# Kernel tuning notes

Measured on AMD Instinct MI355X. Metric: run time of the kernel, lower is better.

Reference implementation:

```python
import jax, jax.numpy as jnp
import numpy as np

M = 41
RHO = 4.0
HDIM = 10
NMODES = 2
BATCH = 16384


def triplet_index(m_size, rho):
    # reduced PBC triplet index set: n >= m, |m|,|n|,|m+n| <= (M-1)/2, |m*n| <= rho*(M-1)/2
    h = (m_size - 1) // 2
    idx = [(m, n) for m in range(-h, h + 1) for n in range(m, h + 1)
           if abs(m + n) <= h and abs(m * n) <= rho * h]
    return np.array(idx, dtype=np.int32)

IDX = triplet_index(M, RHO)
S = len(IDX)


def _c(a):
    # last-dim-2 real tensor -> complex
    return jax.lax.complex(a[..., 0], a[..., 1])


def setup_inputs() -> dict:
    key = jax.random.key(0)
    ks = jax.random.split(key, 6)
    x = jax.random.normal(ks[0], (BATCH, M, NMODES, 2), dtype=jnp.float32)
    task_info = jax.random.uniform(ks[1], (BATCH, 4), dtype=jnp.float32)  # col 0 = power in dBm
    pbc_C = 0.01 * jax.random.normal(ks[2], (S, 2), dtype=jnp.float32)  # complex PBC coeffs
    W1 = jax.random.normal(ks[3], (HDIM, NMODES, S, 2), dtype=jnp.float32) / np.sqrt(2.0 * NMODES * S)
    b1 = jnp.zeros((HDIM, 2), dtype=jnp.float32)
    W2 = jax.random.normal(ks[4], (HDIM, NMODES, M, 2), dtype=jnp.float32) / np.sqrt(2.0 * NMODES * M)
    b2 = jnp.zeros((HDIM, 2), dtype=jnp.float32)
    m_idx = jnp.asarray(IDX[:, 0], dtype=jnp.int32)
    n_idx = jnp.asarray(IDX[:, 1], dtype=jnp.int32)
    return {"x": x, "task_info": task_info, "pbc_C": pbc_C,
            "W1": W1, "b1": b1, "W2": W2, "b2": b2,
            "m_idx": m_idx, "n_idx": n_idx}


def _nonlinear_features(E, m_idx, n_idx):
    # E: [B, M, 2] complex -> [B, 2, S]; Manakov dual-pol triplets:
    # F[p] = (E[c+m,p]*conj(E[c+m+n,p]) + E[c+m,q]*conj(E[c+m+n,q])) * E[c+n,p]
    c = E.shape[1] // 2
    A = E[:, c + m_idx, :] * jnp.conj(E[:, c + m_idx + n_idx, :])  # [B, S, 2]
    F = (A + A[..., ::-1]) * E[:, c + n_idx, :]                    # [B, S, 2]
    return jnp.transpose(F, (0, 2, 1))                             # [B, 2, S]


def _conv_full(Wc, bc, inp):
    # ComplexConv1d whose kernel spans the whole input length (output length 1) -> [B, out]
    return jnp.einsum('oik,bik->bo', Wc, inp) + bc


def _forward(x, task_info, pbc_C, W1, b1, W2, b2, m_idx, n_idx):
    E = _c(x)                                    # [B, M, 2] complex64
    c = M // 2
    P = 10.0 ** (task_info[:, 0] / 10.0) / NMODES  # [B] launch power per mode
    F = _nonlinear_features(E, m_idx, n_idx)     # [B, 2, S]
    # EqAMPBC: center symbol + P * (triplet features . complex coeffs)
    pbc_out = E[:, c, :] + P[:, None] * jnp.einsum('bps,s->bp', F, _c(pbc_C))  # [B, 2]
    w1, bb1, w2, bb2 = _c(W1), _c(b1), _c(W2), _c(b2)
    # A = cat([f1(fo), f1(fo with pols flipped)], dim=-1) -> [B, hdim, 2]
    A = jnp.stack([_conv_full(w1, bb1, F), _conv_full(w1, bb1, F[:, ::-1, :])], axis=-1)
    Et = jnp.transpose(E, (0, 2, 1))             # [B, 2, M]
    Bm = jnp.stack([_conv_full(w2, bb2, Et), _conv_full(w2, bb2, Et[:, ::-1, :])], axis=-1)
    term = jnp.sum(A * Bm * jnp.conj(Bm) + jnp.conj(A) * Bm * Bm, axis=1)  # [B, 2]
    out = pbc_out + (1e-4 / np.sqrt(HDIM)) * term * (P[:, None] ** 2)
    return jnp.stack([out.real, out.imag], axis=-1)  # [B, 2, 2] float32


def reference(x, task_info, pbc_C, W1, b1, W2, b2, m_idx, n_idx):
    return _forward(x, task_info, pbc_C, W1, b1, W2, b2, m_idx, n_idx)
```

## Files before the change

### kernel.cpp

```cpp
#include <hip/hip_runtime.h>
#include <hip/hip_bf16.h>

typedef short bf16x8 __attribute__((ext_vector_type(8)));
typedef float f32x16 __attribute__((ext_vector_type(16)));
typedef float f32x4  __attribute__((ext_vector_type(4)));
typedef float f32x2  __attribute__((ext_vector_type(2)));

#define NCOL  32
#define KS1   112
#define KS2   12
#define ESTR  528

#define WP_OFF   0
#define W2P_OFF  229376

#define MET_OFF  21648
#define SUM_OFF  25360
#define SUM2_OFF 41744
#define LDS_BYTES 58128

__device__ __forceinline__ unsigned short f2bf(float f) {
    union { float f; unsigned u; } v; v.f = f;
    unsigned r = v.u + 0x7FFFu + ((v.u >> 16) & 1u);
    return (unsigned short)(r >> 16);
}
__device__ __forceinline__ unsigned pk2(float a, float b) {
    __hip_bfloat162 h = __float22bfloat162_rn(make_float2(a, b));
    unsigned u; __builtin_memcpy(&u, &h, 4); return u;
}
__device__ __forceinline__ bf16x8 asbf(uint4 v) {
    union { uint4 u; bf16x8 b; } z; z.u = v; return z.b;
}
__device__ __forceinline__ f32x16 zero16() {
    f32x16 z;
#pragma unroll
    for (int i = 0; i < 16; ++i) z[i] = 0.f;
    return z;
}

__global__ void prep_kernel(const float* __restrict__ W1,
                            const float* __restrict__ W2,
                            const float* __restrict__ pbcC,
                            unsigned short* __restrict__ Wp,
                            unsigned short* __restrict__ W2p, int S) {
    int idx = blockIdx.x * 256 + threadIdx.x;
    const int N1 = KS1 * 2 * 64 * 2;
    const int N2 = KS2 * 2 * 64 * 2;
    if (idx < N1) {
        int ks = idx >> 8, rem = idx & 255;
        int mt = rem >> 7; rem &= 127;
        int lane = rem >> 1, jh = rem & 1;
        int row = mt * 32 + (lane & 31);
        int kg  = ks * 16 + (lane >> 5) * 8 + jh * 4;
        int s   = kg >> 2;
        float2 wj0 = make_float2(0.f, 0.f), wj1 = make_float2(0.f, 0.f);
        int p = 0, r = 0;
        if (s < S) {
            if (row < 40) {
                int o = row >> 2; p = (row >> 1) & 1; r = row & 1;
                wj0 = ((const float2*)W1)[(size_t)(o * 2 + 0) * S + s];
                wj1 = ((const float2*)W1)[(size_t)(o * 2 + 1) * S + s];
            } else if (row < 44) {
                p = (row >> 1) & 1; r = row & 1;
                wj0 = ((const float2*)pbcC)[s];
            }
        }
        ushort4 h; unsigned short us[4];
#pragma unroll
        for (int t = 0; t < 4; ++t) {
            int i = t & 1, cc = t >> 1, j2 = i ^ p;
            float2 w = j2 ? wj1 : wj0;
            float v = (cc == 0) ? (r ? w.y : w.x) : (r ? w.x : -w.y);
            us[t] = f2bf(v);
        }
        h.x = us[0]; h.y = us[1]; h.z = us[2]; h.w = us[3];
        ((ushort4*)Wp)[idx] = h;
        return;
    }
    idx -= N1;
    if (idx < N2) {
        int ks = idx >> 8, rem = idx & 255;
        int mt = rem >> 7; rem &= 127;
        int lane = rem >> 1, jh = rem & 1;
        int row = mt * 32 + (lane & 31);
        int kg  = ks * 16 + (lane >> 5) * 8 + jh * 4;
        int m   = kg >> 2;
        float2 wj0 = make_float2(0.f, 0.f), wj1 = make_float2(0.f, 0.f);
        int p = 0, r = 0;
        if (m < 41 && row < 40) {
            int o = row >> 2; p = (row >> 1) & 1; r = row & 1;
            wj0 = ((const float2*)W2)[(o * 2 + 0) * 41 + m];
            wj1 = ((const float2*)W2)[(o * 2 + 1) * 41 + m];
        }
        ushort4 h; unsigned short us[4];
#pragma unroll
        for (int t = 0; t < 4; ++t) {
            int i = t & 1, cc = t >> 1, j2 = i ^ p;
            float2 w = j2 ? wj1 : wj0;
            float v = (cc == 0) ? (r ? w.y : w.x) : (r ? w.x : -w.y);
            us[t] = f2bf(v);
        }
        h.x = us[0]; h.y = us[1]; h.z = us[2]; h.w = us[3];
        ((ushort4*)W2p)[idx] = h;
    }
}

__global__ __launch_bounds__(512, 4) void eqsonn_kernel(
    const float* __restrict__ x, const float* __restrict__ task,
    const unsigned short* __restrict__ Wp,
    const unsigned short* __restrict__ W2p,
    const int* __restrict__ m_idx, const int* __restrict__ n_idx,
    const float* __restrict__ b1, const float* __restrict__ b2,
    float* __restrict__ out, int B, int S)
{
    __shared__ alignas(16) char ldsb[LDS_BYTES];
    const int tid  = threadIdx.x;
    const int lane = tid & 63;
    const int w    = __builtin_amdgcn_readfirstlane(tid >> 6);
    const int col  = lane & 31;
    const int kha  = lane >> 5;
    const int b0   = blockIdx.x * NCOL;

    for (int e = tid; e < 41 * NCOL; e += 512) {
        int bb = e / 41, k = e - bb * 41;
        int bs = b0 + bb; if (bs > B - 1) bs = B - 1;
        float4 v = ((const float4*)x)[(size_t)bs * 41 + k];
        f32x4 pv; pv.x = v.x; pv.y = v.z; pv.z = v.y; pv.w = v.w;
        *(f32x4*)(ldsb + k * ESTR + bb * 16) = pv;
    }
    if (tid < 464) {
        int m = 0, n = 0;
        if (tid < S) { m = m_idx[tid]; n = n_idx[tid]; }
        unsigned offM = (unsigned)((20 + m) * ESTR);
        unsigned offB = (unsigned)((20 + m + n) * ESTR);
        unsigned offN = (unsigned)((20 + n) * ESTR);
        *(uint2*)(ldsb + MET_OFF + tid * 8) = make_uint2(offM | (offB << 16), offN);
    }
    __syncthreads();

    const char* Ebase = ldsb + col * 16;
    auto ldM4 = [&](int ks) -> uint4 {
        return *(const uint4*)(ldsb + MET_OFF + (ks * 4 + kha * 2) * 8);
    };
    auto ldE = [&](unsigned off) -> f32x4 {
        return *(const f32x4*)(Ebase + off);
    };
    auto fbuild = [&](f32x4 em, f32x4 eq, f32x4 en, unsigned& lo, unsigned& hi) {
        f32x2 mr = em.xy, mi = em.zw;
        f32x2 qr = eq.xy, qi = eq.zw;
        f32x2 nr = en.xy, ni = en.zw;
        f32x2 t = mr * qr + mi * qi;
        f32x2 u = mi * qr - mr * qi;
        float sr = t.x + t.y, si = u.x + u.y;
        f32x2 Fr = sr * nr - si * ni;
        f32x2 Fi = sr * ni + si * nr;
        lo = pk2(Fr.x, Fr.y); hi = pk2(Fi.x, Fi.y);
    };

    f32x16 ac0 = zero16(), ac1 = zero16();
    {
        const int ks0 = w * 14;
        const short* Wp16 = (const short*)Wp;
        uint4 M = ldM4(ks0);
        f32x4 e0 = ldE(M.x & 0xffffu), e1 = ldE(M.x >> 16), e2 = ldE(M.y);
        f32x4 e3 = ldE(M.z & 0xffffu), e4 = ldE(M.z >> 16), e5 = ldE(M.w);
        uint4 Mc = ldM4(ks0 + 1);
        const short* ap0 = Wp16 + (size_t)ks0 * 1024 + lane * 8;
        bf16x8 A0 = *(const bf16x8*)(ap0);
        bf16x8 A1 = *(const bf16x8*)(ap0 + 512);
        for (int ks = ks0; ks < ks0 + 14; ++ks) {
            int ksn = (ks + 1 < KS1) ? ks + 1 : KS1 - 1;
            const short* apn = Wp16 + (size_t)ksn * 1024 + lane * 8;
            bf16x8 N0 = *(const bf16x8*)(apn);
            bf16x8 N1 = *(const bf16x8*)(apn + 512);
            f32x4 f0 = ldE(Mc.x & 0xffffu), f1v = ldE(Mc.x >> 16), f2v = ldE(Mc.y);
            f32x4 f3 = ldE(Mc.z & 0xffffu), f4v = ldE(Mc.z >> 16), f5v = ldE(Mc.w);
            uint4 Mn = ldM4(ks + 2);
            unsigned g0, g1, g2, g3;
            fbuild(e0, e1, e2, g0, g1);
            fbuild(e3, e4, e5, g2, g3);
            bf16x8 bfr = asbf(make_uint4(g0, g1, g2, g3));
            ac0 = __builtin_amdgcn_mfma_f32_32x32x16_bf16(A0, bfr, ac0, 0, 0, 0);
            ac1 = __builtin_amdgcn_mfma_f32_32x32x16_bf16(A1, bfr, ac1, 0, 0, 0);
            e0 = f0; e1 = f1v; e2 = f2v; e3 = f3; e4 = f4v; e5 = f5v; Mc = Mn;
            A0 = N0; A1 = N1;
        }
    }

    f32x16 bc0 = zero16(), bc1 = zero16();
    {
        const short* W216 = (const short*)W2p;
        for (int ks2 = w; ks2 < KS2; ks2 += 8) {
            const short* ap = W216 + (size_t)ks2 * 1024 + lane * 8;
            bf16x8 A0 = *(const bf16x8*)(ap);
            bf16x8 A1 = *(const bf16x8*)(ap + 512);
            unsigned g[4];
#pragma unroll
            for (int j = 0; j < 2; ++j) {
                int m = ks2 * 4 + kha * 2 + j;
                int mc = m < 41 ? m : 40;
                f32x4 v = *(const f32x4*)(ldsb + mc * ESTR + col * 16);
                unsigned lo = pk2(v.x, v.y);
                unsigned hi = pk2(v.z, v.w);
                if (m >= 41) { lo = 0u; hi = 0u; }
                g[j * 2] = lo; g[j * 2 + 1] = hi;
            }
            bf16x8 bfr = asbf(make_uint4(g[0], g[1], g[2], g[3]));
            bc0 = __builtin_amdgcn_mfma_f32_32x32x16_bf16(A0, bfr, bc0, 0, 0, 0);
            bc1 = __builtin_amdgcn_mfma_f32_32x32x16_bf16(A1, bfr, bc1, 0, 0, 0);
        }
    }

    float* Reg = (float*)(ldsb + ((w < 4) ? SUM_OFF : SUM2_OFF));
    const int ph = w & 3;
    auto dump = [&](f32x16 a, int baserow, bool add) {
#pragma unroll
        for (int reg = 0; reg < 16; ++reg) {
            int row = baserow + (reg & 3) + 8 * (reg >> 2) + 4 * kha;
            int idx = row * 32 + col;
            if (add) Reg[idx] += a[reg]; else Reg[idx] = a[reg];
        }
    };
    for (int p = 0; p < 4; ++p) {
        if (ph == p) {
            bool add = (p != 0);
            dump(ac0, 0, add); dump(ac1, 32, add);
            dump(bc0, 64, add); dump(bc1, 96, add);
        }
        __syncthreads();
    }

    {
        float4* S1 = (float4*)(ldsb + SUM_OFF);
        float4* S2 = (float4*)(ldsb + SUM2_OFF);
#pragma unroll
        for (int i = 0; i < 2; ++i) {
            int idx = tid + i * 512;
            float4 a = S1[idx], b = S2[idx];
            a.x += b.x; a.y += b.y; a.z += b.z; a.w += b.w;
            S1[idx] = a;
        }
    }
    __syncthreads();

    if (w == 0 && lane < NCOL) {
        const float* Sum = (const float*)(ldsb + SUM_OFF);
        int c = lane;
        float pr0 = Sum[40 * 32 + c], pi0 = Sum[41 * 32 + c];
        float pr1 = Sum[42 * 32 + c], pi1 = Sum[43 * 32 + c];
        float t0 = 0.f, t1 = 0.f, t2 = 0.f, t3 = 0.f;
#pragma unroll
        for (int o = 0; o < 10; ++o) {
            float b2r = b2[o * 2], b2i = b2[o * 2 + 1];
            float b1r = b1[o * 2], b1i = b1[o * 2 + 1];
            int rb = o * 4;
            float B0r = Sum[(64 + rb + 0) * 32 + c] + b2r;
            float B0i = Sum[(64 + rb + 1) * 32 + c] + b2i;
            float B1r = Sum[(64 + rb + 2) * 32 + c] + b2r;
            float B1i = Sum[(64 + rb + 3) * 32 + c] + b2i;
            float A0r = Sum[(rb + 0) * 32 + c] + b1r;
            float A0i = Sum[(rb + 1) * 32 + c] + b1i;
            float A1r = Sum[(rb + 2) * 32 + c] + b1r;
            float A1i = Sum[(rb + 3) * 32 + c] + b1i;
            float g0 = 2.f * (A0r * B0r + A0i * B0i);
            t0 += g0 * B0r; t1 += g0 * B0i;
            float g1 = 2.f * (A1r * B1r + A1i * B1i);
            t2 += g1 * B1r; t3 += g1 * B1i;
        }
        int b = b0 + c;
        if (b < B) {
            float dbm = task[(size_t)b * 4];
            float P   = exp2f(dbm * 0.33219280948873623f) * 0.5f;
            float kP2 = 3.1622776601683794e-05f * P * P;
            float4 Ec = ((const float4*)x)[(size_t)b * 41 + 20];
            float4 o4;
            o4.x = Ec.x + P * pr0 + kP2 * t0;
            o4.y = Ec.y + P * pi0 + kP2 * t1;
            o4.z = Ec.z + P * pr1 + kP2 * t2;
            o4.w = Ec.w + P * pi1 + kP2 * t3;
            ((float4*)out)[b] = o4;
        }
    }
}

extern "C" void kernel_launch(void* const* d_in, const int* in_sizes, int n_in,
                              void* d_out, int out_size, void* d_ws, size_t ws_size,
                              hipStream_t stream) {
    const float* x     = (const float*)d_in[0];
    const float* task  = (const float*)d_in[1];
    const float* pbcC  = (const float*)d_in[2];
    const float* W1    = (const float*)d_in[3];
    const float* b1    = (const float*)d_in[4];
    const float* W2    = (const float*)d_in[5];
    const float* b2    = (const float*)d_in[6];
    const int*   m_idx = (const int*)d_in[7];
    const int*   n_idx = (const int*)d_in[8];
    float* out = (float*)d_out;

    int S = in_sizes[7];
    int B = in_sizes[0] / (41 * 2 * 2);

    char* ws = (char*)d_ws;
    unsigned short* Wp  = (unsigned short*)(ws + WP_OFF);
    unsigned short* W2p = (unsigned short*)(ws + W2P_OFF);

    int prep_n = KS1 * 2 * 64 * 2 + KS2 * 2 * 64 * 2;
    prep_kernel<<<(prep_n + 255) / 256, 256, 0, stream>>>(W1, W2, pbcC, Wp, W2p, S);

    int grid = (B + NCOL - 1) / NCOL;
    eqsonn_kernel<<<grid, 512, 0, stream>>>(x, task, Wp, W2p, m_idx, n_idx,
                                            b1, b2, out, B, S);
}
```

Baseline: 90.30 us.

## Replace phased LDS reduction with atomic adds and deepen weight prefetch

Swaps the four-phase serialized LDS dump (with a barrier per phase and a second partial buffer) for LDS float atomicAdd into one zero-initialised sum buffer. Only the accumulator rows that are consumed are added. The weight prefetch in the main MFMA loop is deepened from one to two steps ahead, and the clamp/zero masking in the W2 stage is removed. The goal is fewer barriers, less LDS and better latency hiding, at the cost of atomic contention and the W2 loop reading unmasked rows past index 40.

New measurement: 149.0 us. 1.65x slower.

```diff
diff --git a/kernel.cpp b/kernel.cpp
--- a/kernel.cpp
+++ b/kernel.cpp
@@ -16,8 +16,7 @@
 
 #define MET_OFF  21648
 #define SUM_OFF  25360
-#define SUM2_OFF 41744
-#define LDS_BYTES 58128
+#define LDS_BYTES 41744
 
 __device__ __forceinline__ unsigned short f2bf(float f) {
     union { float f; unsigned u; } v; v.f = f;
@@ -120,6 +119,7 @@
     const int col  = lane & 31;
     const int kha  = lane >> 5;
     const int b0   = blockIdx.x * NCOL;
+    float* SumF = (float*)(ldsb + SUM_OFF);
 
     for (int e = tid; e < 41 * NCOL; e += 512) {
         int bb = e / 41, k = e - bb * 41;
@@ -127,6 +127,11 @@
         float4 v = ((const float4*)x)[(size_t)bs * 41 + k];
         f32x4 pv; pv.x = v.x; pv.y = v.z; pv.z = v.y; pv.w = v.w;
         *(f32x4*)(ldsb + k * ESTR + bb * 16) = pv;
+    }
+    {
+        float4 z4 = make_float4(0.f, 0.f, 0.f, 0.f);
+        float4* Z = (float4*)(ldsb + SUM_OFF);
+        Z[tid] = z4; Z[tid + 512] = z4;
     }
     if (tid < 464) {
         int m = 0, n = 0;
@@ -168,11 +173,14 @@
         const short* ap0 = Wp16 + (size_t)ks0 * 1024 + lane * 8;
         bf16x8 A0 = *(const bf16x8*)(ap0);
         bf16x8 A1 = *(const bf16x8*)(ap0 + 512);
+        const short* ap1 = Wp16 + (size_t)(ks0 + 1) * 1024 + lane * 8;
+        bf16x8 B0 = *(const bf16x8*)(ap1);
+        bf16x8 B1 = *(const bf16x8*)(ap1 + 512);
         for (int ks = ks0; ks < ks0 + 14; ++ks) {
-            int ksn = (ks + 1 < KS1) ? ks + 1 : KS1 - 1;
+            int ksn = (ks + 2 < KS1) ? ks + 2 : KS1 - 1;
             const short* apn = Wp16 + (size_t)ksn * 1024 + lane * 8;
-            bf16x8 N0 = *(const bf16x8*)(apn);
-            bf16x8 N1 = *(const bf16x8*)(apn + 512);
+            bf16x8 C0 = *(const bf16x8*)(apn);
+            bf16x8 C1 = *(const bf16x8*)(apn + 512);
             f32x4 f0 = ldE(Mc.x & 0xffffu), f1v = ldE(Mc.x >> 16), f2v = ldE(Mc.y);
             f32x4 f3 = ldE(Mc.z & 0xffffu), f4v = ldE(Mc.z >> 16), f5v = ldE(Mc.w);
             uint4 Mn = ldM4(ks + 2);
@@ -183,9 +191,20 @@
             ac0 = __builtin_amdgcn_mfma_f32_32x32x16_bf16(A0, bfr, ac0, 0, 0, 0);
             ac1 = __builtin_amdgcn_mfma_f32_32x32x16_bf16(A1, bfr, ac1, 0, 0, 0);
             e0 = f0; e1 = f1v; e2 = f2v; e3 = f3; e4 = f4v; e5 = f5v; Mc = Mn;
-            A0 = N0; A1 = N1;
-        }
-    }
+            A0 = B0; A1 = B1; B0 = C0; B1 = C1;
+        }
+    }
+
+    auto dumpat = [&](f32x16 a, int baserow, int nregs) {
+#pragma unroll
+        for (int reg = 0; reg < 16; ++reg) {
+            if (reg >= nregs) break;
+            int row = baserow + (reg & 3) + 8 * (reg >> 2) + 4 * kha;
+            atomicAdd(&SumF[row * 32 + col], a[reg]);
+        }
+    };
+    dumpat(ac0, 0, 16);
+    dumpat(ac1, 32, 8);
 
     f32x16 bc0 = zero16(), bc1 = zero16();
     {
@@ -198,53 +217,21 @@
 #pragma unroll
             for (int j = 0; j < 2; ++j) {
                 int m = ks2 * 4 + kha * 2 + j;
-                int mc = m < 41 ? m : 40;
-                f32x4 v = *(const f32x4*)(ldsb + mc * ESTR + col * 16);
-                unsigned lo = pk2(v.x, v.y);
-                unsigned hi = pk2(v.z, v.w);
-                if (m >= 41) { lo = 0u; hi = 0u; }
-                g[j * 2] = lo; g[j * 2 + 1] = hi;
+                f32x4 v = *(const f32x4*)(ldsb + m * ESTR + col * 16);
+                g[j * 2]     = pk2(v.x, v.y);
+                g[j * 2 + 1] = pk2(v.z, v.w);
             }
             bf16x8 bfr = asbf(make_uint4(g[0], g[1], g[2], g[3]));
             bc0 = __builtin_amdgcn_mfma_f32_32x32x16_bf16(A0, bfr, bc0, 0, 0, 0);
             bc1 = __builtin_amdgcn_mfma_f32_32x32x16_bf16(A1, bfr, bc1, 0, 0, 0);
         }
     }
-
-    float* Reg = (float*)(ldsb + ((w < 4) ? SUM_OFF : SUM2_OFF));
-    const int ph = w & 3;
-    auto dump = [&](f32x16 a, int baserow, bool add) {
-#pragma unroll
-        for (int reg = 0; reg < 16; ++reg) {
-            int row = baserow + (reg & 3) + 8 * (reg >> 2) + 4 * kha;
-            int idx = row * 32 + col;
-            if (add) Reg[idx] += a[reg]; else Reg[idx] = a[reg];
-        }
-    };
-    for (int p = 0; p < 4; ++p) {
-        if (ph == p) {
-            bool add = (p != 0);
-            dump(ac0, 0, add); dump(ac1, 32, add);
-            dump(bc0, 64, add); dump(bc1, 96, add);
-        }
-        __syncthreads();
-    }
-
-    {
-        float4* S1 = (float4*)(ldsb + SUM_OFF);
-        float4* S2 = (float4*)(ldsb + SUM2_OFF);
-#pragma unroll
-        for (int i = 0; i < 2; ++i) {
-            int idx = tid + i * 512;
-            float4 a = S1[idx], b = S2[idx];
-            a.x += b.x; a.y += b.y; a.z += b.z; a.w += b.w;
-            S1[idx] = a;
-        }
-    }
+    dumpat(bc0, 64, 16);
+    dumpat(bc1, 96, 4);
     __syncthreads();
 
     if (w == 0 && lane < NCOL) {
-        const float* Sum = (const float*)(ldsb + SUM_OFF);
+        const float* Sum = SumF;
         int c = lane;
         float pr0 = Sum[40 * 32 + c], pi0 = Sum[41 * 32 + c];
         float pr1 = Sum[42 * 32 + c], pi1 = Sum[43 * 32 + c];
```
